# Performance work log

Measured on AMD Instinct MI355X. Metric: run time of the kernel, lower is better.

## Reference

```python
import jax, jax.numpy as jnp
import numpy as np
import math

HIDDEN = 2048
N_HEADS = 16
HEAD_DIM = HIDDEN // N_HEADS  # 128
ROPE_THETA = 10000.0


def _rope_cos_sin(seq_len, dim, theta, dtype):
    # Megatron RotaryEmbedding: freqs = pos \outer inv_freq; emb = cat(freqs, freqs)
    inv_freq = 1.0 / (theta ** (jnp.arange(0, dim, 2, dtype=jnp.float32) / dim))
    pos = jnp.arange(seq_len, dtype=jnp.float32)
    freqs = jnp.outer(pos, inv_freq)            # [S, dim/2]
    emb = jnp.concatenate([freqs, freqs], -1)   # [S, dim]
    return jnp.cos(emb).astype(dtype), jnp.sin(emb).astype(dtype)


def _rotate_half(x):
    half = x.shape[-1] // 2
    return jnp.concatenate([-x[..., half:], x[..., :half]], axis=-1)


def setup_inputs() -> dict:
    key = jax.random.key(0)
    k1, k2, k3 = jax.random.split(key, 3)
    B, S = 2, 2048
    hidden_states = jax.random.normal(k1, (B, S, HIDDEN), dtype=jnp.float32)
    # torch Linear weights are [out_features, in_features]
    w_qkv = jax.random.normal(k2, (3 * HIDDEN, HIDDEN), dtype=jnp.float32) * (1.0 / math.sqrt(HIDDEN))
    w_o = jax.random.normal(k3, (HIDDEN, HIDDEN), dtype=jnp.float32) * (1.0 / math.sqrt(HIDDEN))
    return {"hidden_states": hidden_states, "w_qkv": w_qkv, "w_o": w_o}


def reference(hidden_states, w_qkv, w_o):
    B, S, H = hidden_states.shape
    # fused QKV projection: [B,S,H] @ [H, 3H] -> view (.., n_heads, 3, head_dim)
    mixed = jnp.einsum('bsh,oh->bso', hidden_states, w_qkv)
    mixed = mixed.reshape(B, S, N_HEADS, 3, HEAD_DIM)
    q, k, v = mixed[..., 0, :], mixed[..., 1, :], mixed[..., 2, :]  # [B,S,Hn,D]

    # fused split + RoPE (full rotary dim = head_dim)
    cos, sin = _rope_cos_sin(S, HEAD_DIM, ROPE_THETA, hidden_states.dtype)
    cos = cos[None, :, None, :]  # [1,S,1,D]
    sin = sin[None, :, None, :]
    q = q * cos + _rotate_half(q) * sin
    k = k * cos + _rotate_half(k) * sin

    # causal scaled-dot-product attention (flash_attn_func equivalent math)
    scale = 1.0 / math.sqrt(HEAD_DIM)
    scores = jnp.einsum('bqhd,bkhd->bhqk', q, k) * scale  # [B,Hn,S,S]
    causal = jnp.tril(jnp.ones((S, S), dtype=bool))
    scores = jnp.where(causal[None, None], scores, jnp.finfo(scores.dtype).min)
    probs = jax.nn.softmax(scores, axis=-1)
    attn = jnp.einsum('bhqk,bkhd->bqhd', probs, v)  # [B,S,Hn,D]

    attn = attn.reshape(B, S, H)
    out = jnp.einsum('bsh,oh->bso', attn, w_o)
    return out
```

## Files before the change

### kernel.cpp

```cpp
#include <hip/hip_runtime.h>
#include <hip/hip_bf16.h>
#include <cstdint>
#include <cstddef>

#define S_DIM 2048
#define H_DIM 2048
#define NHEAD 16
#define HD_DIM 128
#define O3    6144
#define BS    4096
#define NBH   32

typedef short  s16x4  __attribute__((ext_vector_type(4)));
typedef short  s16x8  __attribute__((ext_vector_type(8)));
typedef __bf16 bf16x8 __attribute__((ext_vector_type(8)));
typedef float  f32x4  __attribute__((ext_vector_type(4)));

__device__ __forceinline__ unsigned short f2bf(float f) {
  unsigned int b = __float_as_uint(f);
  b += 0x7FFFu + ((b >> 16) & 1u);
  return (unsigned short)(b >> 16);
}
__device__ __forceinline__ float bf2f(unsigned short u) {
  return __uint_as_float(((unsigned int)u) << 16);
}
__device__ __forceinline__ bf16x8 load8(const unsigned short* p) {
  s16x8 r = *(const s16x8*)p;
  return __builtin_bit_cast(bf16x8, r);
}
__device__ __forceinline__ f32x4 mfma_bf16(bf16x8 a, bf16x8 b, f32x4 c) {
  return __builtin_amdgcn_mfma_f32_16x16x32_bf16(a, b, c, 0, 0, 0);
}
__device__ __forceinline__ void gload_lds16(const void* g, void* l) {
  __builtin_amdgcn_global_load_lds(
      (__attribute__((address_space(1))) unsigned int*)g,
      (__attribute__((address_space(3))) unsigned int*)l, 16, 0, 0);
}

__global__ void prep_kernel(const float* __restrict__ hid,
                            const float* __restrict__ wqkv,
                            const float* __restrict__ wo,
                            unsigned short* __restrict__ hid_b,
                            unsigned short* __restrict__ wqkv_b,
                            unsigned short* __restrict__ wo_b,
                            float* __restrict__ cosT,
                            float* __restrict__ sinT) {
  const int nA = 2097152, nB = 3145728, nC = 1048576, nD = 131072;
  const int total = nA + nB + nC + nD;
  int stride = gridDim.x * blockDim.x;
  for (int i = blockIdx.x * blockDim.x + threadIdx.x; i < total; i += stride) {
    if (i < nA + nB + nC) {
      const float* src; unsigned short* dst; int j;
      if (i < nA)            { src = hid;  dst = hid_b;  j = i; }
      else if (i < nA + nB)  { src = wqkv; dst = wqkv_b; j = i - nA; }
      else                   { src = wo;   dst = wo_b;   j = i - nA - nB; }
      float4 v = ((const float4*)src)[j];
      ushort4 o;
      o.x = f2bf(v.x); o.y = f2bf(v.y); o.z = f2bf(v.z); o.w = f2bf(v.w);
      ((ushort4*)dst)[j] = o;
    } else {
      int idx = i - nA - nB - nC;
      int s = idx >> 6, d = idx & 63;
      float inv = expf(-((float)d / 64.0f) * 9.210340371976184f);
      float ang = (float)s * inv;
      float sn, cs;
      sincosf(ang, &sn, &cs);
      cosT[idx] = cs;
      sinT[idx] = sn;
    }
  }
}

template <bool OUT_BF16, bool QKV_MAP>
__global__ __launch_bounds__(512, 1)
void gemm3b_kernel(const unsigned short* __restrict__ A,
                   const unsigned short* __restrict__ Bw,
                   void* __restrict__ C, int M, int N, int K) {
  __shared__ __align__(16) unsigned short lA[3][128 * 64];
  __shared__ __align__(16) unsigned short lB[3][256 * 64];
  const int tid  = threadIdx.x;
  const int wave = tid >> 6, lane = tid & 63;
  const int wm = wave >> 2, wn = wave & 3;
  const int lg = lane >> 4, ll = lane & 15;

  const int nbx = gridDim.x;
  const int id  = blockIdx.y * nbx + blockIdx.x;
  int m_tile, n_tile;
  if (QKV_MAP) {
    const int k = id & 7, q = id >> 3;
    const int ng = q >> 5, r = q & 31;
    m_tile = (k >> 1) * 8 + (r & 7);
    n_tile = (k & 1) * 12 + ng * 4 + (r >> 3);
  } else {
    const int nwg = gridDim.x * gridDim.y;
    const int swz = (id & 7) * (nwg >> 3) + (id >> 3);
    m_tile = swz / nbx;
    n_tile = swz % nbx;
  }
  const int m0 = m_tile * 128, n0 = n_tile * 256;

  f32x4 acc[4][4];
#pragma unroll
  for (int i = 0; i < 4; ++i)
#pragma unroll
    for (int j = 0; j < 4; ++j) acc[i][j] = (f32x4){0.f, 0.f, 0.f, 0.f};

  const unsigned short* aP[2];
  const unsigned short* bP[4];
  int aD[2], bD[4];
#pragma unroll
  for (int i = 0; i < 2; ++i) {
    int cb = (i * 8 + wave) * 64 + lane;
    int cs = cb ^ ((cb >> 3) & 7);
    aP[i] = A + (size_t)(m0 + (cs >> 3)) * K + (cs & 7) * 8;
    aD[i] = cb * 8;
  }
#pragma unroll
  for (int i = 0; i < 4; ++i) {
    int cb = (i * 8 + wave) * 64 + lane;
    int cs = cb ^ ((cb >> 3) & 7);
    bP[i] = Bw + (size_t)(n0 + (cs >> 3)) * K + (cs & 7) * 8;
    bD[i] = cb * 8;
  }

  auto STAGE = [&](int buf, int t) {
    const int kt = t << 6;
#pragma unroll
    for (int i = 0; i < 2; ++i) gload_lds16(aP[i] + kt, &lA[buf][aD[i]]);
#pragma unroll
    for (int i = 0; i < 4; ++i) gload_lds16(bP[i] + kt, &lB[buf][bD[i]]);
  };

  const int NT = K >> 6;
  STAGE(0, 0);
  if (NT > 1) {
    STAGE(1, 1);
    asm volatile("s_waitcnt vmcnt(6)" ::: "memory");
  } else {
    asm volatile("s_waitcnt vmcnt(0)" ::: "memory");
  }
  asm volatile("s_barrier" ::: "memory");

  for (int t = 0; t < NT; ++t) {
    const int cur = t % 3;
    const char* lAc = (const char*)&lA[cur][0];
    const char* lBc = (const char*)&lB[cur][0];

    bf16x8 af[4][2], bfr[2][2][2];
#pragma unroll
    for (int fq = 0; fq < 4; ++fq) {
      int r = wm * 64 + fq * 16 + ll;
#pragma unroll
      for (int kk = 0; kk < 2; ++kk) {
        int a = (r * 128 + kk * 64 + lg * 16) ^ ((r & 7) << 4);
        af[fq][kk] = load8((const unsigned short*)(lAc + a));
      }
    }
#pragma unroll
    for (int nh = 0; nh < 2; ++nh)
#pragma unroll
      for (int fq = 0; fq < 2; ++fq) {
        int r = wn * 64 + nh * 32 + fq * 16 + ll;
#pragma unroll
        for (int kk = 0; kk < 2; ++kk) {
          int a = (r * 128 + kk * 64 + lg * 16) ^ ((r & 7) << 4);
          bfr[nh][fq][kk] = load8((const unsigned short*)(lBc + a));
        }
      }

    if (t + 2 < NT) STAGE((t + 2) % 3, t + 2);

    __builtin_amdgcn_s_setprio(1);
#pragma unroll
    for (int nh = 0; nh < 2; ++nh)
#pragma unroll
      for (int fq = 0; fq < 4; ++fq)
#pragma unroll
        for (int gq = 0; gq < 2; ++gq)
#pragma unroll
          for (int kk = 0; kk < 2; ++kk)
            acc[fq][nh * 2 + gq] =
                mfma_bf16(af[fq][kk], bfr[nh][gq][kk], acc[fq][nh * 2 + gq]);
    __builtin_amdgcn_s_setprio(0);

    if (t + 2 < NT)
      asm volatile("s_waitcnt vmcnt(6)" ::: "memory");
    else if (t + 1 < NT)
      asm volatile("s_waitcnt vmcnt(0)" ::: "memory");
    asm volatile("s_barrier" ::: "memory");
  }

#pragma unroll
  for (int fm = 0; fm < 4; ++fm)
#pragma unroll
    for (int fn = 0; fn < 4; ++fn)
#pragma unroll
      for (int j = 0; j < 4; ++j) {
        int r   = m0 + wm * 64 + fm * 16 + lg * 4 + j;
        int col = n0 + wn * 64 + fn * 16 + ll;
        if (OUT_BF16)
          ((unsigned short*)C)[(size_t)r * N + col] = f2bf(acc[fm][fn][j]);
        else
          ((float*)C)[(size_t)r * N + col] = acc[fm][fn][j];
      }
}

__global__ void rope_qk_kernel(const unsigned short* __restrict__ mixed,
                               const float* __restrict__ cosT,
                               const float* __restrict__ sinT,
                               unsigned short* __restrict__ qr,
                               unsigned short* __restrict__ kr) {
  int m = blockIdx.x;
  int s = m & (S_DIM - 1);
  int b = m >> 11;
  const unsigned short* row = mixed + (size_t)m * O3;
  int t = threadIdx.x;
  int h = t >> 4, dg = (t & 15) << 2;
  int base = h * 384;
  s16x4 q0 = *(const s16x4*)(row + base + dg);
  s16x4 q1 = *(const s16x4*)(row + base + 64 + dg);
  s16x4 k0 = *(const s16x4*)(row + base + 128 + dg);
  s16x4 k1 = *(const s16x4*)(row + base + 192 + dg);
  float4 c4 = *(const float4*)(cosT + (s << 6) + dg);
  float4 s4 = *(const float4*)(sinT + (s << 6) + dg);
  size_t ob = ((size_t)(b * NHEAD + h) * S_DIM + s) * HD_DIM;
  s16x4 oq0, oq1, ok0, ok1;
  float cc[4] = {c4.x, c4.y, c4.z, c4.w};
  float ss[4] = {s4.x, s4.y, s4.z, s4.w};
#pragma unroll
  for (int i = 0; i < 4; ++i) {
    float q0f = bf2f((unsigned short)q0[i]), q1f = bf2f((unsigned short)q1[i]);
    float k0f = bf2f((unsigned short)k0[i]), k1f = bf2f((unsigned short)k1[i]);
    oq0[i] = (short)f2bf(q0f * cc[i] - q1f * ss[i]);
    oq1[i] = (short)f2bf(q1f * cc[i] + q0f * ss[i]);
    ok0[i] = (short)f2bf(k0f * cc[i] - k1f * ss[i]);
    ok1[i] = (short)f2bf(k1f * cc[i] + k0f * ss[i]);
  }
  *(s16x4*)(qr + ob + dg)      = oq0;
  *(s16x4*)(qr + ob + 64 + dg) = oq1;
  *(s16x4*)(kr + ob + dg)      = ok0;
  *(s16x4*)(kr + ob + 64 + dg) = ok1;
}

__global__ __launch_bounds__(256)
void vtrans_kernel(const unsigned short* __restrict__ mixed,
                   unsigned short* __restrict__ vt) {
  __shared__ unsigned short t[64 * 65];
  int st = blockIdx.x, dt = blockIdx.y, bh = blockIdx.z;
  int b = bh >> 4, h = bh & 15;
  int s0 = st * 64, d0 = dt * 64;
  int tid = threadIdx.x;
#pragma unroll
  for (int it = 0; it < 2; ++it) {
    int c = it * 256 + tid;
    int sl = c >> 3, dc = c & 7;
    const unsigned short* src =
        mixed + (size_t)(b * S_DIM + s0 + sl) * O3 + h * 384 + 256 + d0 + dc * 8;
    s16x8 v = *(const s16x8*)src;
#pragma unroll
    for (int i = 0; i < 8; ++i) t[(dc * 8 + i) * 65 + sl] = (unsigned short)v[i];
  }
  __syncthreads();
#pragma unroll
  for (int it = 0; it < 2; ++it) {
    int c = it * 256 + tid;
    int dl = c >> 3, sc = c & 7;
    s16x8 v;
#pragma unroll
    for (int i = 0; i < 8; ++i) v[i] = (short)t[dl * 65 + sc * 8 + i];
    *(s16x8*)(vt + ((size_t)bh * HD_DIM + d0 + dl) * S_DIM + s0 + sc * 8) = v;
  }
}

__global__ __launch_bounds__(512, 1)
void attn_kernel(const unsigned short* __restrict__ qr,
                 const unsigned short* __restrict__ kr,
                 const unsigned short* __restrict__ vt,
                 unsigned short* __restrict__ out) {
  __shared__ __align__(16) unsigned short kbuf[2][64 * 128];
  __shared__ __align__(16) unsigned short vbuf[2][128 * 64];
  __shared__ __align__(16) unsigned short plds[8][16 * 72];
  const int p = blockIdx.x, bh = blockIdx.y;
  const int wave = threadIdx.x >> 6, lane = threadIdx.x & 63;
  const int b = bh >> 4, h = bh & 15;
  const int lg = lane >> 4, ll = lane & 15;
  const unsigned short* Qb = qr + (size_t)bh * S_DIM * HD_DIM;
  const unsigned short* Kb = kr + (size_t)bh * S_DIM * HD_DIM;
  const unsigned short* Vb = vt + (size_t)bh * HD_DIM * S_DIM;
  const float kE  = 0.12752792f;
  const float THR = 11.5416f;
  unsigned short* pw = &plds[wave][0];

  for (int seg = 0; seg < 2; ++seg) {
    const int qt = seg ? (15 - p) : p;
    const int qbase = qt * 128 + wave * 16;
    const int ntb = 2 * qt + 2;

    auto STAGE = [&](int buf, int t) {
      const int k0 = t * 64;
#pragma unroll
      for (int i = 0; i < 2; ++i) {
        int cb = (i * 8 + wave) * 64;
        int c  = cb + lane;
        int cs = c ^ ((c >> 4) & 7);
        gload_lds16(Kb + (size_t)(k0 + (cs >> 4)) * HD_DIM + (cs & 15) * 8,
                    &kbuf[buf][cb * 8]);
      }
#pragma unroll
      for (int i = 0; i < 2; ++i) {
        int cb = (i * 8 + wave) * 64;
        int c  = cb + lane;
        int cv = c ^ ((c >> 3) & 7);
        gload_lds16(Vb + (size_t)(cv >> 3) * S_DIM + k0 + (cv & 7) * 8,
                    &vbuf[buf][cb * 8]);
      }
    };

    bf16x8 aq[4];
#pragma unroll
    for (int kk = 0; kk < 4; ++kk)
      aq[kk] = load8(Qb + (size_t)(qbase + ll) * HD_DIM + kk * 32 + lg * 8);

    float mk[4], lsum[4];
    f32x4 o[8];
#pragma unroll
    for (int j = 0; j < 4; ++j) { mk[j] = -1e30f; lsum[j] = 0.f; }
#pragma unroll
    for (int f = 0; f < 8; ++f) o[f] = (f32x4){0.f, 0.f, 0.f, 0.f};

    STAGE(0, 0);
    __syncthreads();

    for (int t = 0; t < ntb; ++t) {
      const int cur = t & 1;
      if (t + 1 < ntb) STAGE(cur ^ 1, t + 1);
      const int k0 = t * 64;
      const bool maskt = (t >= ntb - 2);

      f32x4 s[4];
#pragma unroll
      for (int kf = 0; kf < 4; ++kf) s[kf] = (f32x4){0.f, 0.f, 0.f, 0.f};
      const char* kb = (const char*)&kbuf[cur][0];
      __builtin_amdgcn_s_setprio(1);
#pragma unroll
      for (int kf = 0; kf < 4; ++kf) {
        int r = kf * 16 + ll;
#pragma unroll
        for (int kk = 0; kk < 4; ++kk) {
          int a = (r * 256 + kk * 64 + lg * 16) ^ ((r & 7) << 4);
          s[kf] = mfma_bf16(aq[kk], load8((const unsigned short*)(kb + a)), s[kf]);
        }
      }
      __builtin_amdgcn_s_setprio(0);

      if (maskt) {
#pragma unroll
        for (int kf = 0; kf < 4; ++kf) {
          int kcol = k0 + kf * 16 + ll;
#pragma unroll
          for (int j = 0; j < 4; ++j) {
            int qrow = qbase + lg * 4 + j;
            if (kcol > qrow) s[kf][j] = -1e31f;
          }
        }
      }

      float pmax[4];
      bool ok = true;
#pragma unroll
      for (int j = 0; j < 4; ++j) {
        pmax[j] = fmaxf(fmaxf(s[0][j], s[1][j]), fmaxf(s[2][j], s[3][j]));
        ok = ok && (pmax[j] * kE - mk[j] <= THR);
      }
      if (!__all(ok)) {
#pragma unroll
        for (int j = 0; j < 4; ++j) {
          float rm = pmax[j] * kE;
#pragma unroll
          for (int off = 1; off < 16; off <<= 1)
            rm = fmaxf(rm, __shfl_xor(rm, off, 64));
          rm = fmaxf(rm, mk[j]);
          float corr = exp2f(mk[j] - rm);
          mk[j] = rm;
          lsum[j] *= corr;
#pragma unroll
          for (int f = 0; f < 8; ++f) o[f][j] *= corr;
        }
      }
#pragma unroll
      for (int j = 0; j < 4; ++j) {
        int prow = (lg * 4 + j) * 72;
#pragma unroll
        for (int kf = 0; kf < 4; ++kf) {
          float e = exp2f(fmaf(s[kf][j], kE, -mk[j]));
          lsum[j] += e;
          pw[prow + kf * 16 + ll] = f2bf(e);
        }
      }

      bf16x8 pa0 = load8(&pw[ll * 72 + lg * 8]);
      bf16x8 pa1 = load8(&pw[ll * 72 + 32 + lg * 8]);
      const char* vb = (const char*)&vbuf[cur][0];
      __builtin_amdgcn_s_setprio(1);
#pragma unroll
      for (int f = 0; f < 8; ++f) {
        int rv = f * 16 + ll;
        int a0 = (rv * 128 + lg * 16) ^ ((rv & 7) << 4);
        int a1 = (rv * 128 + 64 + lg * 16) ^ ((rv & 7) << 4);
        o[f] = mfma_bf16(pa0, load8((const unsigned short*)(vb + a0)), o[f]);
        o[f] = mfma_bf16(pa1, load8((const unsigned short*)(vb + a1)), o[f]);
      }
      __builtin_amdgcn_s_setprio(0);

      __syncthreads();
    }

#pragma unroll
    for (int j = 0; j < 4; ++j) {
      float l = lsum[j];
#pragma unroll
      for (int off = 1; off < 16; off <<= 1) l += __shfl_xor(l, off, 64);
      lsum[j] = 1.0f / l;
    }
#pragma unroll
    for (int f = 0; f < 8; ++f)
#pragma unroll
      for (int j = 0; j < 4; ++j) {
        int srow = qbase + lg * 4 + j;
        out[((size_t)(b * S_DIM + srow)) * H_DIM + h * HD_DIM + f * 16 + ll] =
            f2bf(o[f][j] * lsum[j]);
      }
  }
}

extern "C" void kernel_launch(void* const* d_in, const int* in_sizes, int n_in,
                              void* d_out, int out_size, void* d_ws, size_t ws_size,
                              hipStream_t stream) {
  (void)in_sizes; (void)n_in; (void)out_size; (void)ws_size;
  const float* hidden = (const float*)d_in[0];
  const float* wqkv   = (const float*)d_in[1];
  const float* wo     = (const float*)d_in[2];
  char* ws = (char*)d_ws;
  unsigned short* hid_b  = (unsigned short*)(ws);
  unsigned short* wqkv_b = (unsigned short*)(ws + 16777216);
  unsigned short* wo_b   = (unsigned short*)(ws + 41943040);
  unsigned short* mixed  = (unsigned short*)(ws + 50331648);
  unsigned short* q_r    = (unsigned short*)(ws + 100663296);
  unsigned short* k_r    = (unsigned short*)(ws + 117440512);
  unsigned short* v_t    = (unsigned short*)(ws + 134217728);
  unsigned short* attn   = (unsigned short*)(ws + 150994944);
  float* cosT            = (float*)(ws + 167772160);
  float* sinT            = (float*)(ws + 168296448);

  prep_kernel<<<2048, 256, 0, stream>>>(hidden, wqkv, wo, hid_b, wqkv_b, wo_b,
                                        cosT, sinT);

  gemm3b_kernel<true, true><<<dim3(O3 / 256, BS / 128), 512, 0, stream>>>(
      hid_b, wqkv_b, mixed, BS, O3, H_DIM);

  rope_qk_kernel<<<BS, 256, 0, stream>>>(mixed, cosT, sinT, q_r, k_r);
  vtrans_kernel<<<dim3(32, 2, 32), 256, 0, stream>>>(mixed, v_t);

  attn_kernel<<<dim3(8, 32), 512, 0, stream>>>(q_r, k_r, v_t, attn);

  gemm3b_kernel<false, false><<<dim3(H_DIM / 256, BS / 128), 512, 0, stream>>>(
      attn, wo_b, d_out, BS, H_DIM, H_DIM);
}
```

Before: 264.2 us.

## Use 256x256-tile ping-pong GEMM with XCD swizzle for QKV projection

Replaces the 128x256 triple-buffered QKV GEMM with a new 256x256 tile kernel that double-buffers LDS in two k-halves. It interleaves the global-to-LDS prefetch with MFMA phases using barriers and setprio, and remaps workgroups round-robin across 8 XCDs. The aim is higher arithmetic intensity per tile and better overlap of loads with matrix math. The trade-off is half as many workgroups (384), which could underfill 256 CUs, and the previous QKV-specific tile mapping is dropped.

```diff
diff --git a/kernel.cpp b/kernel.cpp
--- a/kernel.cpp
+++ b/kernel.cpp
@@ -71,6 +71,125 @@
   }
 }
 
+__global__ __launch_bounds__(512, 1)
+void gemm256p_kernel(const unsigned short* __restrict__ A,
+                     const unsigned short* __restrict__ Bw,
+                     unsigned short* __restrict__ C, int M, int N, int K) {
+  __shared__ __align__(16) unsigned short lA[2][2][8192];
+  __shared__ __align__(16) unsigned short lB[2][2][8192];
+  const int tid  = threadIdx.x;
+  const int wave = tid >> 6, lane = tid & 63;
+  const int wm = wave >> 2, wn = wave & 3;
+  const int lg = lane >> 4, ll = lane & 15;
+
+  const int nbx = gridDim.x;
+  const int nwg = gridDim.x * gridDim.y;
+  const int id  = blockIdx.y * nbx + blockIdx.x;
+  const int swz = (id & 7) * (nwg >> 3) + (id >> 3);
+  const int m0 = (swz / nbx) * 256, n0 = (swz % nbx) * 256;
+
+  f32x4 acc[8][4];
+#pragma unroll
+  for (int i = 0; i < 8; ++i)
+#pragma unroll
+    for (int j = 0; j < 4; ++j) acc[i][j] = (f32x4){0.f, 0.f, 0.f, 0.f};
+
+  const unsigned short* aSrc[2];
+  const unsigned short* bSrc[2];
+  int dOff[2];
+#pragma unroll
+  for (int i = 0; i < 2; ++i) {
+    int cb = i * 512 + tid;
+    int cs = cb ^ ((cb >> 3) & 3);
+    int row = cs >> 2, kc = cs & 3;
+    aSrc[i] = A + (size_t)(m0 + row) * K + kc * 8;
+    bSrc[i] = Bw + (size_t)(n0 + row) * K + kc * 8;
+    dOff[i] = cb * 8;
+  }
+  auto STG_A = [&](int buf, int kkh, int kt) {
+#pragma unroll
+    for (int i = 0; i < 2; ++i)
+      gload_lds16(aSrc[i] + kt + kkh * 32, &lA[buf][kkh][dOff[i]]);
+  };
+  auto STG_B = [&](int buf, int kkh, int kt) {
+#pragma unroll
+    for (int i = 0; i < 2; ++i)
+      gload_lds16(bSrc[i] + kt + kkh * 32, &lB[buf][kkh][dOff[i]]);
+  };
+
+  const int NT = K >> 6;
+  STG_A(0, 0, 0); STG_B(0, 0, 0); STG_A(0, 1, 0); STG_B(0, 1, 0);
+  asm volatile("s_waitcnt vmcnt(4)" ::: "memory");
+  asm volatile("s_barrier" ::: "memory");
+
+  for (int t = 0; t < NT; ++t) {
+    const int buf = t & 1, nbuf = buf ^ 1;
+    const int ktn = (t + 1) << 6;
+    const bool st = (t + 1 < NT);
+    bf16x8 af[8], bf[2];
+
+#pragma unroll
+    for (int kk = 0; kk < 2; ++kk) {
+      const unsigned short* la = &lA[buf][kk][0];
+      const unsigned short* lb = &lB[buf][kk][0];
+#pragma unroll
+      for (int fm = 0; fm < 8; ++fm) {
+        int r = wm * 128 + fm * 16 + ll;
+        af[fm] = load8(la + r * 32 + (lg ^ ((r >> 1) & 3)) * 8);
+      }
+#pragma unroll
+      for (int gq = 0; gq < 2; ++gq) {
+        int r = wn * 64 + gq * 16 + ll;
+        bf[gq] = load8(lb + r * 32 + (lg ^ ((r >> 1) & 3)) * 8);
+      }
+      if (st) { if (kk == 0) STG_A(nbuf, 0, ktn); else STG_A(nbuf, 1, ktn); }
+      asm volatile("s_barrier" ::: "memory");
+      asm volatile("s_waitcnt lgkmcnt(0)" ::: "memory");
+      __builtin_amdgcn_sched_barrier(0);
+      __builtin_amdgcn_s_setprio(1);
+#pragma unroll
+      for (int fm = 0; fm < 8; ++fm)
+#pragma unroll
+        for (int gq = 0; gq < 2; ++gq)
+          acc[fm][gq] = mfma_bf16(af[fm], bf[gq], acc[fm][gq]);
+      __builtin_amdgcn_s_setprio(0);
+      __builtin_amdgcn_sched_barrier(0);
+      asm volatile("s_barrier" ::: "memory");
+
+#pragma unroll
+      for (int gq = 0; gq < 2; ++gq) {
+        int r = wn * 64 + (2 + gq) * 16 + ll;
+        bf[gq] = load8(lb + r * 32 + (lg ^ ((r >> 1) & 3)) * 8);
+      }
+      if (st) { if (kk == 0) STG_B(nbuf, 0, ktn); else STG_B(nbuf, 1, ktn); }
+      asm volatile("s_barrier" ::: "memory");
+      asm volatile("s_waitcnt lgkmcnt(0)" ::: "memory");
+      __builtin_amdgcn_sched_barrier(0);
+      __builtin_amdgcn_s_setprio(1);
+#pragma unroll
+      for (int fm = 0; fm < 8; ++fm)
+#pragma unroll
+        for (int gq = 0; gq < 2; ++gq)
+          acc[fm][2 + gq] = mfma_bf16(af[fm], bf[gq], acc[fm][2 + gq]);
+      __builtin_amdgcn_s_setprio(0);
+      __builtin_amdgcn_sched_barrier(0);
+      asm volatile("s_waitcnt vmcnt(4)" ::: "memory");
+      asm volatile("s_barrier" ::: "memory");
+    }
+  }
+
+#pragma unroll
+  for (int fm = 0; fm < 8; ++fm)
+#pragma unroll
+    for (int fn = 0; fn < 4; ++fn)
+#pragma unroll
+      for (int j = 0; j < 4; ++j) {
+        int r   = m0 + wm * 128 + fm * 16 + lg * 4 + j;
+        int col = n0 + wn * 64 + fn * 16 + ll;
+        C[(size_t)r * N + col] = f2bf(acc[fm][fn][j]);
+      }
+}
+
 template <bool OUT_BF16, bool QKV_MAP>
 __global__ __launch_bounds__(512, 1)
 void gemm3b_kernel(const unsigned short* __restrict__ A,
@@ -455,7 +574,7 @@
   prep_kernel<<<2048, 256, 0, stream>>>(hidden, wqkv, wo, hid_b, wqkv_b, wo_b,
                                         cosT, sinT);
 
-  gemm3b_kernel<true, true><<<dim3(O3 / 256, BS / 128), 512, 0, stream>>>(
+  gemm256p_kernel<<<dim3(O3 / 256, BS / 256), 512, 0, stream>>>(
       hid_b, wqkv_b, mixed, BS, O3, H_DIM);
 
   rope_qk_kernel<<<BS, 256, 0, stream>>>(mixed, cosT, sinT, q_r, k_r);
```

Measured after the change: 284.0 us. +7.5%, slower.
